# Kernel optimization log

Measured on AMD Instinct MI355X. Metric: run time of the kernel, lower is better.

Reference implementation:

```python
import jax, jax.numpy as jnp
import numpy as np

B = 32768
H = 512
NH = 8
EPS = 1e-5


def _glorot(key, shape):
    fan_in, fan_out = shape[-1], shape[0]
    lim = (6.0 / (fan_in + fan_out)) ** 0.5
    return jax.random.uniform(key, shape, jnp.float32, -lim, lim)


def setup_inputs() -> dict:
    key = jax.random.key(0)
    ks = jax.random.split(key, 32)
    d = {
        "graph_features": jax.random.normal(ks[0], (B, H), jnp.float32),
        "seq_features": jax.random.normal(ks[1], (B, H), jnp.float32),
        "tabular_features": jax.random.normal(ks[2], (B, H), jnp.float32),
    }
    i = 3
    for name in ("g2s", "s2g", "t2m"):
        d[f"{name}_w_in"] = _glorot(ks[i], (3 * H, H)); i += 1
        d[f"{name}_b_in"] = jnp.zeros((3 * H,), jnp.float32)
        d[f"{name}_w_out"] = _glorot(ks[i], (H, H)); i += 1
        d[f"{name}_b_out"] = jnp.zeros((H,), jnp.float32)
    for name in ("gate_g", "gate_s", "gate_t"):
        d[f"{name}_w"] = _glorot(ks[i], (H, 2 * H)); i += 1
        d[f"{name}_b"] = jnp.zeros((H,), jnp.float32)
    d["fc1_w"] = _glorot(ks[i], (2 * H, 3 * H)); i += 1
    d["fc1_b"] = jnp.zeros((2 * H,), jnp.float32)
    d["ln_g"] = jnp.ones((2 * H,), jnp.float32)
    d["ln_b"] = jnp.zeros((2 * H,), jnp.float32)
    d["fc2_w"] = _glorot(ks[i], (H, 2 * H)); i += 1
    d["fc2_b"] = jnp.zeros((H,), jnp.float32)
    return d


def _mha(q, k, v, w_in, b_in, w_out, b_out):
    # q: [B,Sq,H], k/v: [B,Sk,H]. PyTorch nn.MultiheadAttention math (eval mode).
    dh = H // NH
    qp = q @ w_in[:H].T + b_in[:H]
    kp = k @ w_in[H:2 * H].T + b_in[H:2 * H]
    vp = v @ w_in[2 * H:].T + b_in[2 * H:]
    qh = qp.reshape(qp.shape[0], qp.shape[1], NH, dh)
    kh = kp.reshape(kp.shape[0], kp.shape[1], NH, dh)
    vh = vp.reshape(vp.shape[0], vp.shape[1], NH, dh)
    scores = jnp.einsum("bqhd,bkhd->bhqk", qh, kh) / jnp.sqrt(jnp.float32(dh))
    attn = jax.nn.softmax(scores, axis=-1)
    out = jnp.einsum("bhqk,bkhd->bqhd", attn, vh).reshape(q.shape[0], q.shape[1], H)
    return out @ w_out.T + b_out


def reference(graph_features, seq_features, tabular_features,
              g2s_w_in, g2s_b_in, g2s_w_out, g2s_b_out,
              s2g_w_in, s2g_b_in, s2g_w_out, s2g_b_out,
              t2m_w_in, t2m_b_in, t2m_w_out, t2m_b_out,
              gate_g_w, gate_g_b, gate_s_w, gate_s_b, gate_t_w, gate_t_b,
              fc1_w, fc1_b, ln_g, ln_b, fc2_w, fc2_b):
    g = graph_features[:, None, :]   # [B,1,H]
    s = seq_features[:, None, :]
    t = tabular_features[:, None, :]

    graph_to_seq = _mha(s, g, g, g2s_w_in, g2s_b_in, g2s_w_out, g2s_b_out)
    seq_to_graph = _mha(g, s, s, s2g_w_in, s2g_b_in, s2g_w_out, s2g_b_out)

    graph_gate = jax.nn.sigmoid(jnp.concatenate([g, seq_to_graph], -1) @ gate_g_w.T + gate_g_b)
    seq_gate = jax.nn.sigmoid(jnp.concatenate([s, graph_to_seq], -1) @ gate_s_w.T + gate_s_b)
    gated_graph = g * graph_gate
    gated_seq = s * seq_gate

    multimodal = jnp.concatenate([gated_graph, gated_seq], axis=1)  # [B,2,H]
    t2m = _mha(multimodal, t, t, t2m_w_in, t2m_b_in, t2m_w_out, t2m_b_out)  # [B,2,H]

    tab_comb = jnp.concatenate([t, t2m.mean(axis=1, keepdims=True)], -1)
    tab_gate = jax.nn.sigmoid(tab_comb @ gate_t_w.T + gate_t_b)
    gated_tab = t * tab_gate

    allf = jnp.concatenate([gated_graph[:, 0], gated_seq[:, 0], gated_tab[:, 0]], -1)  # [B,3H]
    h = allf @ fc1_w.T + fc1_b
    mu = h.mean(-1, keepdims=True)
    var = ((h - mu) ** 2).mean(-1, keepdims=True)
    h = (h - mu) / jnp.sqrt(var + EPS) * ln_g + ln_b
    h = jax.nn.relu(h)
    return h @ fc2_w.T + fc2_b
```

## Files before the change

### kernel.cpp

```cpp
#include <hip/hip_runtime.h>
#include <stdint.h>
#include <stddef.h>

#define MROWS 32768
#define HDIM  512
#define CH    16384
#define BM 128
#define BN 128
#define BK 64

typedef __attribute__((ext_vector_type(8))) _Float16 half8;
typedef __attribute__((ext_vector_type(4))) _Float16 half4v;
typedef __attribute__((ext_vector_type(4))) float    f32x4;

static __device__ __forceinline__ void gld_lds16(const void* g, void* l) {
    __builtin_amdgcn_global_load_lds(
        (__attribute__((address_space(1))) void*)(uintptr_t)g,
        (__attribute__((address_space(3))) void*)(uint32_t)(uintptr_t)l,
        16, 0, 0);
}

struct CvtJob  { const float* src; _Float16* dst; int srcld4, dstld, rowlen4, rows; };
struct CvtJobs { CvtJob j[11]; };

__global__ __launch_bounds__(256)
void cvt_rows(CvtJobs J) {
    const CvtJob jb = J.j[blockIdx.y];
    const int row = blockIdx.x;
    if (row >= jb.rows) return;
    const float4* __restrict__ s = (const float4*)jb.src + (size_t)row * jb.srcld4;
    _Float16* __restrict__ d = jb.dst + (size_t)row * jb.dstld;
    for (int c = threadIdx.x; c < jb.rowlen4; c += 256) {
        const float4 v = s[c];
        half4v o = { (_Float16)v.x, (_Float16)v.y, (_Float16)v.z, (_Float16)v.w };
        *(half4v*)(d + c * 4) = o;
    }
}

__global__ __launch_bounds__(384)
void cvt_chunk3(const float* __restrict__ x0, const float* __restrict__ x1,
                const float* __restrict__ x2, _Float16* __restrict__ dst) {
    const int row = blockIdx.x;
    const int mod = threadIdx.x >> 7;
    const int c   = threadIdx.x & 127;
    const float* s = (mod == 0) ? x0 : (mod == 1) ? x1 : x2;
    const float4 v = ((const float4*)(s + (size_t)row * 512))[c];
    half4v o = { (_Float16)v.x, (_Float16)v.y, (_Float16)v.z, (_Float16)v.w };
    *(half4v*)(dst + (size_t)row * 1536 + mod * 512 + c * 4) = o;
}

struct TcvtArgs { const float* src[3]; _Float16* dst; };
__global__ __launch_bounds__(256)
void tcvt512(TcvtArgs a) {
    __shared__ float t[32][33];
    const int m = blockIdx.z;
    const float* __restrict__ src = a.src[m];
    _Float16* __restrict__ dst = a.dst + (size_t)m * HDIM * HDIM;
    const int bx = blockIdx.x * 32, by = blockIdx.y * 32;
    const int tx = threadIdx.x & 31, ty = threadIdx.x >> 5;
    #pragma unroll
    for (int q = 0; q < 4; ++q)
        t[ty + q * 8][tx] = src[(size_t)(by + ty + q * 8) * 512 + bx + tx];
    __syncthreads();
    #pragma unroll
    for (int q = 0; q < 4; ++q)
        dst[(size_t)(bx + ty + q * 8) * 512 + by + tx] = (_Float16)t[tx][ty + q * 8];
}

struct MvArgs { const float* W[3]; const float* x[3]; const float* b[3]; float* y; int ldw, woff; };
__global__ __launch_bounds__(256)
void mv3(MvArgs a) {
    const int m = blockIdx.y;
    const int i = blockIdx.x * 256 + threadIdx.x;
    const float* __restrict__ W = a.W[m] + (size_t)i * a.ldw + a.woff;
    const float* __restrict__ x = a.x[m];
    float s = a.b[m][i];
    for (int j = 0; j < 512; ++j) s += W[j] * x[j];
    a.y[m * 512 + i] = s;
}

struct GemmP {
    const void* A1;
    const _Float16* W; const float* bias; void* C;
    int K, ldA1, ldw, ldc, coff;
    int zsA, zsW, zsC;
    const void* A1b; const _Float16* Wb; const float* biasb;
    int Kb, ldwb, coffb, nyb;
};

template<int EPI, int OCC, int MERGED>
__global__ __launch_bounds__(256, OCC)
void gemm_k(GemmP p) {
    __shared__ __align__(16) unsigned char smem[32768];
    _Float16* Asm = (_Float16*)smem;
    _Float16* Bsm = (_Float16*)(smem + 16384);

    const int tid  = threadIdx.x;
    const int wid  = tid >> 6;
    const int lane = tid & 63;
    const int m0 = blockIdx.x * BM;
    const int n0 = blockIdx.y * BN;

    const _Float16* __restrict__ A1h;
    const _Float16* __restrict__ Wp;
    const float* biasp;
    char* Cz;
    int K, ldA1, ldw, coff;
    if (MERGED && blockIdx.z == 1) {
        if ((int)blockIdx.y >= p.nyb) return;
        A1h = (const _Float16*)p.A1b; Wp = p.Wb; biasp = p.biasb;
        Cz = (char*)p.C; K = p.Kb; ldA1 = p.ldA1; ldw = p.ldwb; coff = p.coffb;
    } else {
        const ptrdiff_t zz = MERGED ? 0 : (ptrdiff_t)blockIdx.z;
        A1h = (const _Float16*)((const char*)p.A1 + zz * p.zsA);
        Wp  = (const _Float16*)((const char*)p.W + zz * p.zsW);
        biasp = p.bias;
        Cz = (char*)p.C + zz * p.zsC;
        K = p.K; ldA1 = p.ldA1; ldw = p.ldw; coff = p.coff;
    }

    const int wr = (wid >> 1) * 64;
    const int wc = (wid & 1) * 64;
    const int l15 = lane & 15;
    const int lhi = lane >> 4;

    f32x4 acc[4][4] = {};
    half8 xsave[8];
    const int colsel = (tid & 15) * 8;
    const int xtile  = n0 + (colsel & 64);
    const int xco    = colsel & 63;

    for (int kt = 0; kt < K; kt += BK) {
        #pragma unroll
        for (int i = 0; i < 4; ++i) {
            const int seg = wid * 256 + i * 64 + lane;
            const int row = seg >> 3;
            const int ke  = (seg & 7) * 8;
            gld_lds16(Wp  + (size_t)(n0 + row) * ldw  + kt + ke, &Bsm[seg * 8]);
            gld_lds16(A1h + (size_t)(m0 + row) * ldA1 + kt + ke, &Asm[seg * 8]);
        }
        __syncthreads();
        if (EPI == 1 && kt == xtile) {
            #pragma unroll
            for (int q = 0; q < 8; ++q)
                xsave[q] = *(const half8*)&Asm[(q * 16 + (tid >> 4)) * BK + xco];
        }
        #pragma unroll
        for (int kk = 0; kk < BK; kk += 32) {
            half8 fa[4], fb[4];
            #pragma unroll
            for (int i = 0; i < 4; ++i) {
                fa[i] = *(const half8*)&Asm[(wr + i * 16 + l15) * BK + kk + lhi * 8];
                fb[i] = *(const half8*)&Bsm[(wc + i * 16 + l15) * BK + kk + lhi * 8];
            }
            #pragma unroll
            for (int i = 0; i < 4; ++i)
                #pragma unroll
                for (int j = 0; j < 4; ++j)
                    acc[i][j] = __builtin_amdgcn_mfma_f32_16x16x32_f16(fa[i], fb[j], acc[i][j], 0, 0, 0);
        }
        __syncthreads();
    }

    if (EPI == 3) {
        float* Cf = (float*)smem;
        float* __restrict__ C = (float*)Cz;
        #pragma unroll
        for (int h = 0; h < 2; ++h) {
            if ((wr >> 6) == h) {
                #pragma unroll
                for (int j = 0; j < 4; ++j) {
                    const int col = wc + j * 16 + l15;
                    const float bia = biasp ? biasp[n0 + col] : 0.f;
                    #pragma unroll
                    for (int i = 0; i < 4; ++i)
                        #pragma unroll
                        for (int r = 0; r < 4; ++r)
                            Cf[(i * 16 + lhi * 4 + r) * 128 + col] = acc[i][j][r] + bia;
                }
            }
            __syncthreads();
            #pragma unroll
            for (int pph = 0; pph < 8; ++pph) {
                const int seg = pph * 256 + tid;
                const int row = seg >> 5, cs = seg & 31;
                const float4 v = *(const float4*)&Cf[row * 128 + cs * 4];
                *(float4*)&C[(size_t)(m0 + h * 64 + row) * p.ldc + n0 + cs * 4] = v;
            }
            __syncthreads();
        }
    } else {
        _Float16* Ct = (_Float16*)smem;
        #pragma unroll
        for (int j = 0; j < 4; ++j) {
            const int col = wc + j * 16 + l15;
            const float bia = (EPI == 2) ? 0.f : (biasp ? biasp[n0 + col] : 0.f);
            #pragma unroll
            for (int i = 0; i < 4; ++i)
                #pragma unroll
                for (int r = 0; r < 4; ++r) {
                    float v = acc[i][j][r] + bia;
                    if (EPI == 1) v = 1.f / (1.f + __expf(-v));
                    Ct[(wr + i * 16 + lhi * 4 + r) * 128 + col] = (_Float16)v;
                }
        }
        __syncthreads();
        _Float16* __restrict__ C = (_Float16*)Cz;
        #pragma unroll
        for (int pph = 0; pph < 8; ++pph) {
            const int seg = pph * 256 + tid;
            const int row = seg >> 4, cs = seg & 15;
            half8 hv = *(const half8*)&Ct[row * 128 + cs * 8];
            const size_t cidx = (size_t)(m0 + row) * p.ldc + coff + n0 + cs * 8;
            if (EPI == 1) hv = hv * xsave[pph];
            if (EPI == 2) { const half8 old = *(const half8*)&C[cidx]; hv = hv + old; }
            *(half8*)&C[cidx] = hv;
        }
    }
}

__global__ __launch_bounds__(256)
void ln_relu(const _Float16* __restrict__ hin, _Float16* __restrict__ hout,
             const float* __restrict__ gamma, const float* __restrict__ beta) {
    const int row  = blockIdx.x * 4 + (threadIdx.x >> 6);
    const int lane = threadIdx.x & 63;
    const _Float16* hr = hin + (size_t)row * 1024;
    _Float16* ho = hout + (size_t)row * 1024;
    const half8 v0 = *(const half8*)(hr + lane * 8);
    const half8 v1 = *(const half8*)(hr + 512 + lane * 8);
    float f0[8], f1[8];
    float s = 0.f, s2 = 0.f;
    #pragma unroll
    for (int j = 0; j < 8; ++j) {
        f0[j] = (float)v0[j]; s += f0[j]; s2 += f0[j] * f0[j];
        f1[j] = (float)v1[j]; s += f1[j]; s2 += f1[j] * f1[j];
    }
    #pragma unroll
    for (int off = 32; off > 0; off >>= 1) {
        s  += __shfl_xor(s,  off, 64);
        s2 += __shfl_xor(s2, off, 64);
    }
    const float mean = s * (1.f / 1024.f);
    const float var  = s2 * (1.f / 1024.f) - mean * mean;
    const float rstd = rsqrtf(var + 1e-5f);
    half8 o0, o1;
    #pragma unroll
    for (int j = 0; j < 8; ++j) {
        const int i0 = lane * 8 + j, i1 = 512 + lane * 8 + j;
        const float av = (f0[j] - mean) * rstd * gamma[i0] + beta[i0];
        const float bv = (f1[j] - mean) * rstd * gamma[i1] + beta[i1];
        o0[j] = (_Float16)(av > 0.f ? av : 0.f);
        o1[j] = (_Float16)(bv > 0.f ? bv : 0.f);
    }
    *(half8*)(ho + lane * 8) = o0;
    *(half8*)(ho + 512 + lane * 8) = o1;
}

extern "C" void kernel_launch(void* const* d_in, const int* in_sizes, int n_in,
                              void* d_out, int out_size, void* d_ws, size_t ws_size,
                              hipStream_t stream)
{
    (void)in_sizes; (void)n_in; (void)out_size;
    const size_t HH = (size_t)HDIM * HDIM;

    _Float16* wsH   = (_Float16*)d_ws;
    _Float16* slotB = wsH;
    _Float16* Xch   = slotB + (size_t)CH * 1536;
    _Float16* Wouth = Xch   + (size_t)CH * 1536;
    _Float16* Wg2h  = Wouth + 3 * HH;
    _Float16* WvT   = Wg2h  + 3 * HH;
    _Float16* WcoT  = WvT   + 3 * HH;
    _Float16* Wbig  = WcoT  + 3 * HH;
    _Float16* Wc2   = Wbig  + 4 * HH;
    _Float16* fc1h  = Wc2   + 1 * HH;
    _Float16* fc2h  = fc1h  + 6 * HH;
    float*    bco   = (float*)(fc2h + 2 * HH);
    float*    beff  = bco + 3 * 512;
    _Float16* hws   = wsH;
    const size_t need = (size_t)((char*)(beff + 3 * 512) - (char*)d_ws);
    if (ws_size < need) return;

    const float* X[3] = { (const float*)d_in[0], (const float*)d_in[1], (const float*)d_in[2] };
    const int asrc[3] = { 1, 0, 2 };

    CvtJobs cj;
    for (int m = 0; m < 3; ++m) {
        cj.j[m]     = { (const float*)d_in[5 + 4 * m], Wouth + m * HH, 128, 512, 128, 512 };
        cj.j[3 + m] = { (const float*)d_in[15 + 2 * m] + 512, Wg2h + m * HH, 256, 512, 128, 512 };
    }
    cj.j[6]  = { (const float*)d_in[15], Wbig,                    256, 1024, 128, 512 };
    cj.j[7]  = { (const float*)d_in[17], Wbig + 512 * 1024 + 512, 256, 1024, 128, 512 };
    cj.j[8]  = { (const float*)d_in[19], Wc2,                     256, 512,  128, 512 };
    cj.j[9]  = { (const float*)d_in[21], fc1h, 384, 1536, 384, 1024 };
    cj.j[10] = { (const float*)d_in[25], fc2h, 256, 1024, 256, 512 };
    cvt_rows<<<dim3(1024, 11, 1), 256, 0, stream>>>(cj);

    TcvtArgs ta;
    for (int m = 0; m < 3; ++m) ta.src[m] = (const float*)d_in[3 + 4 * m] + 2 * HH;
    ta.dst = WvT;
    tcvt512<<<dim3(16, 16, 3), 256, 0, stream>>>(ta);

    MvArgs mv;
    for (int m = 0; m < 3; ++m) {
        mv.W[m] = (const float*)d_in[5 + 4 * m];
        mv.x[m] = (const float*)d_in[4 + 4 * m] + 2 * HDIM;
        mv.b[m] = (const float*)d_in[6 + 4 * m];
    }
    mv.y = bco; mv.ldw = 512; mv.woff = 0;
    mv3<<<dim3(2, 3, 1), 256, 0, stream>>>(mv);

    GemmP p;
    p.bias = nullptr; p.coff = 0;
    p.zsA = p.zsW = p.zsC = 0;
    p.A1b = nullptr; p.Wb = nullptr; p.biasb = nullptr;
    p.Kb = 0; p.ldwb = 0; p.coffb = 0; p.nyb = 0;

    p.A1 = WvT; p.ldA1 = 512;
    p.W = Wouth; p.ldw = 512;
    p.C = WcoT; p.ldc = 512;
    p.K = 512;
    p.zsA = (int)(HH * 2); p.zsW = (int)(HH * 2); p.zsC = (int)(HH * 2);
    gemm_k<0, 4, 0><<<dim3(4, 4, 3), 256, 0, stream>>>(p);

    p.A1 = Wg2h; p.zsA = (int)(HH * 2);
    p.W = WcoT + HH; p.zsW = -(int)(HH * 2);
    p.C = Wbig + 512; p.ldc = 1024; p.zsC = (int)((512 * 1024 - 512) * 2);
    gemm_k<0, 4, 0><<<dim3(4, 4, 2), 256, 0, stream>>>(p);

    p.A1 = Wg2h + 2 * HH; p.zsA = 0;
    p.W = WcoT + 2 * HH; p.zsW = 0;
    p.C = Wc2; p.ldc = 512; p.zsC = 0;
    gemm_k<2, 4, 0><<<dim3(4, 4, 1), 256, 0, stream>>>(p);

    for (int m = 0; m < 3; ++m) {
        mv.W[m] = (const float*)d_in[15 + 2 * m];
        mv.x[m] = bco + asrc[m] * 512;
        mv.b[m] = (const float*)d_in[16 + 2 * m];
    }
    mv.y = beff; mv.ldw = 1024; mv.woff = 512;
    mv3<<<dim3(2, 3, 1), 256, 0, stream>>>(mv);

    _Float16* hbuf = (_Float16*)d_out;
    for (int c = 0; c < 2; ++c) {
        const size_t roff = (size_t)c * CH;

        cvt_chunk3<<<dim3(CH, 1, 1), 384, 0, stream>>>(
            X[0] + roff * HDIM, X[1] + roff * HDIM, X[2] + roff * HDIM, Xch);

        p.A1 = Xch; p.ldA1 = 1536;
        p.W = Wbig; p.ldw = 1024;
        p.bias = beff;
        p.C = slotB; p.ldc = 1536; p.coff = 0;
        p.K = 1024;
        p.A1b = Xch + 1024; p.Wb = Wc2; p.biasb = beff + 1024;
        p.Kb = 512; p.ldwb = 512; p.coffb = 1024; p.nyb = 4;
        gemm_k<1, 3, 1><<<dim3(CH / BM, 1024 / BN, 2), 256, 0, stream>>>(p);

        p.A1 = slotB; p.ldA1 = 1536;
        p.W = fc1h; p.ldw = 1536;
        p.bias = (const float*)d_in[22];
        p.C = hbuf + roff * 1024; p.ldc = 1024; p.coff = 0;
        p.K = 1536;
        gemm_k<0, 4, 0><<<dim3(CH / BM, 1024 / BN, 1), 256, 0, stream>>>(p);
    }

    ln_relu<<<dim3(MROWS / 4, 1, 1), 256, 0, stream>>>(
        hbuf, hws, (const float*)d_in[23], (const float*)d_in[24]);

    p.A1 = hws; p.ldA1 = 1024;
    p.W = fc2h; p.ldw = 1024;
    p.bias = (const float*)d_in[26];
    p.C = d_out; p.ldc = HDIM; p.coff = 0;
    p.K = 1024;
    gemm_k<3, 4, 0><<<dim3(MROWS / BM, HDIM / BN, 1), 256, 0, stream>>>(p);
}
```

Baseline: 454.1 us.

## Fold next-chunk fp16 conversion into fc1 GEMM grid and flatten merged GEMM grid

The float-to-half conversion of the second row chunk now runs as extra blocks appended to the first chunk's fc1 GEMM launch. This lets it overlap with the GEMM work instead of running as its own serial launch. The merged projection GEMM changes from a z=2 grid, where half the z=1 blocks exited immediately, to a flat 12-column y grid split by a ysplit parameter. The risks are load imbalance from the heavy conversion blocks at the tail, and reliance on Xch no longer being read once the fc1 launch for chunk 0 starts.

```diff
diff --git a/kernel.cpp b/kernel.cpp
--- a/kernel.cpp
+++ b/kernel.cpp
@@ -85,10 +85,11 @@
     int K, ldA1, ldw, ldc, coff;
     int zsA, zsW, zsC;
     const void* A1b; const _Float16* Wb; const float* biasb;
-    int Kb, ldwb, coffb, nyb;
+    int Kb, ldwb, coffb, ysplit;
+    const float *cx0, *cx1, *cx2; _Float16* cdst;
 };
 
-template<int EPI, int OCC, int MERGED>
+template<int EPI, int OCC, int MODE>
 __global__ __launch_bounds__(256, OCC)
 void gemm_k(GemmP p) {
     __shared__ __align__(16) unsigned char smem[32768];
@@ -96,27 +97,42 @@
     _Float16* Bsm = (_Float16*)(smem + 16384);
 
     const int tid  = threadIdx.x;
+
+    if (MODE == 2 && blockIdx.y >= (unsigned)p.ysplit) {
+        const int r0 = blockIdx.x * 128;
+        for (int j = tid; j < 128 * 384; j += 256) {
+            const int r = j / 384;
+            const int t = j - r * 384;
+            const int m = t >> 7, c = t & 127;
+            const float* s = (m == 0) ? p.cx0 : (m == 1 ? p.cx1 : p.cx2);
+            const float4 v = ((const float4*)(s + (size_t)(r0 + r) * 512))[c];
+            half4v o = { (_Float16)v.x, (_Float16)v.y, (_Float16)v.z, (_Float16)v.w };
+            *(half4v*)(p.cdst + (size_t)(r0 + r) * 1536 + m * 512 + c * 4) = o;
+        }
+        return;
+    }
+
     const int wid  = tid >> 6;
     const int lane = tid & 63;
     const int m0 = blockIdx.x * BM;
-    const int n0 = blockIdx.y * BN;
 
     const _Float16* __restrict__ A1h;
     const _Float16* __restrict__ Wp;
     const float* biasp;
     char* Cz;
-    int K, ldA1, ldw, coff;
-    if (MERGED && blockIdx.z == 1) {
-        if ((int)blockIdx.y >= p.nyb) return;
+    int K, ldA1, ldw, coff, n0;
+    if (MODE == 1 && blockIdx.y >= (unsigned)p.ysplit) {
         A1h = (const _Float16*)p.A1b; Wp = p.Wb; biasp = p.biasb;
         Cz = (char*)p.C; K = p.Kb; ldA1 = p.ldA1; ldw = p.ldwb; coff = p.coffb;
+        n0 = (blockIdx.y - p.ysplit) * BN;
     } else {
-        const ptrdiff_t zz = MERGED ? 0 : (ptrdiff_t)blockIdx.z;
+        const ptrdiff_t zz = (MODE == 0) ? (ptrdiff_t)blockIdx.z : 0;
         A1h = (const _Float16*)((const char*)p.A1 + zz * p.zsA);
         Wp  = (const _Float16*)((const char*)p.W + zz * p.zsW);
         biasp = p.bias;
         Cz = (char*)p.C + zz * p.zsC;
         K = p.K; ldA1 = p.ldA1; ldw = p.ldw; coff = p.coff;
+        n0 = blockIdx.y * BN;
     }
 
     const int wr = (wid >> 1) * 64;
@@ -313,7 +329,8 @@
     p.bias = nullptr; p.coff = 0;
     p.zsA = p.zsW = p.zsC = 0;
     p.A1b = nullptr; p.Wb = nullptr; p.biasb = nullptr;
-    p.Kb = 0; p.ldwb = 0; p.coffb = 0; p.nyb = 0;
+    p.Kb = 0; p.ldwb = 0; p.coffb = 0; p.ysplit = 1 << 30;
+    p.cx0 = p.cx1 = p.cx2 = nullptr; p.cdst = nullptr;
 
     p.A1 = WvT; p.ldA1 = 512;
     p.W = Wouth; p.ldw = 512;
@@ -340,12 +357,11 @@
     mv.y = beff; mv.ldw = 1024; mv.woff = 512;
     mv3<<<dim3(2, 3, 1), 256, 0, stream>>>(mv);
 
+    cvt_chunk3<<<dim3(CH, 1, 1), 384, 0, stream>>>(X[0], X[1], X[2], Xch);
+
     _Float16* hbuf = (_Float16*)d_out;
     for (int c = 0; c < 2; ++c) {
         const size_t roff = (size_t)c * CH;
-
-        cvt_chunk3<<<dim3(CH, 1, 1), 384, 0, stream>>>(
-            X[0] + roff * HDIM, X[1] + roff * HDIM, X[2] + roff * HDIM, Xch);
 
         p.A1 = Xch; p.ldA1 = 1536;
         p.W = Wbig; p.ldw = 1024;
@@ -353,15 +369,23 @@
         p.C = slotB; p.ldc = 1536; p.coff = 0;
         p.K = 1024;
         p.A1b = Xch + 1024; p.Wb = Wc2; p.biasb = beff + 1024;
-        p.Kb = 512; p.ldwb = 512; p.coffb = 1024; p.nyb = 4;
-        gemm_k<1, 3, 1><<<dim3(CH / BM, 1024 / BN, 2), 256, 0, stream>>>(p);
+        p.Kb = 512; p.ldwb = 512; p.coffb = 1024; p.ysplit = 8;
+        gemm_k<1, 3, 1><<<dim3(CH / BM, 12, 1), 256, 0, stream>>>(p);
 
         p.A1 = slotB; p.ldA1 = 1536;
         p.W = fc1h; p.ldw = 1536;
         p.bias = (const float*)d_in[22];
         p.C = hbuf + roff * 1024; p.ldc = 1024; p.coff = 0;
-        p.K = 1536;
-        gemm_k<0, 4, 0><<<dim3(CH / BM, 1024 / BN, 1), 256, 0, stream>>>(p);
+        p.K = 1536; p.ysplit = 8;
+        if (c == 0) {
+            p.cx0 = X[0] + (size_t)CH * HDIM;
+            p.cx1 = X[1] + (size_t)CH * HDIM;
+            p.cx2 = X[2] + (size_t)CH * HDIM;
+            p.cdst = Xch;
+            gemm_k<0, 4, 2><<<dim3(CH / BM, 9, 1), 256, 0, stream>>>(p);
+        } else {
+            gemm_k<0, 4, 0><<<dim3(CH / BM, 8, 1), 256, 0, stream>>>(p);
+        }
     }
 
     ln_relu<<<dim3(MROWS / 4, 1, 1), 256, 0, stream>>>(
@@ -371,6 +395,6 @@
     p.W = fc2h; p.ldw = 1024;
     p.bias = (const float*)d_in[26];
     p.C = d_out; p.ldc = HDIM; p.coff = 0;
-    p.K = 1024;
+    p.K = 1024; p.ysplit = 1 << 30;
     gemm_k<3, 4, 0><<<dim3(MROWS / BM, HDIM / BN, 1), 256, 0, stream>>>(p);
 }
```

Result: slower. 529.2 us (+16.5%).
